# Kernel optimization log

Measured on AMD Instinct MI355X. Metric: run time of the kernel, lower is better.

Reference implementation:

```python
import jax, jax.numpy as jnp
import numpy as np

B, N, M, D = 4096, 39, 32, 32   # batch, fields, embed_dim, product_layer_dim
F = 1_000_000                   # features_dim (sparse vocab)
H = [400, 400, 400]             # hidden layer sizes
BN_EPS = 1e-3                   # keras BatchNormalization default epsilon


def setup_inputs() -> dict:
    key = jax.random.key(0)
    ks = jax.random.split(key, 32)
    inp = {
        "feature_index": jax.random.randint(ks[0], (B, N), 0, F),
        "feature_value": jax.random.normal(ks[1], (B, N), dtype=jnp.float32),
        # keras Embedding default 'uniform' initializer: U(-0.05, 0.05)
        "emb_table": jax.random.uniform(ks[2], (F, M), minval=-0.05, maxval=0.05, dtype=jnp.float32),
        "lin_w": jax.random.normal(ks[3], (D, N, M), dtype=jnp.float32) * 0.05,
        "quad_w": jax.random.normal(ks[4], (D, N), dtype=jnp.float32) * 0.1,
    }
    # MLP: input is concat(l_z, l_p) -> 2*D wide
    dims = [2 * D] + H
    k = 5
    for i in range(len(H)):
        fan_in, fan_out = dims[i], dims[i + 1]
        scale = (2.0 / (fan_in + fan_out)) ** 0.5
        inp[f"W{i}"] = jax.random.normal(ks[k], (fan_in, fan_out), dtype=jnp.float32) * scale; k += 1
        inp[f"b{i}"] = jnp.zeros((fan_out,), jnp.float32)
        inp[f"g{i}"] = jnp.ones((fan_out,), jnp.float32)    # BN gamma
        inp[f"be{i}"] = jnp.zeros((fan_out,), jnp.float32)  # BN beta
        inp[f"rm{i}"] = jnp.zeros((fan_out,), jnp.float32)  # BN moving mean
        inp[f"rv{i}"] = jnp.ones((fan_out,), jnp.float32)   # BN moving var
    inp["Wout"] = jax.random.normal(ks[k], (H[-1], 1), dtype=jnp.float32) * 0.05
    inp["bout"] = jnp.zeros((1,), jnp.float32)
    return inp


def _forward(feature_index, emb_table, lin_w, quad_w, layer_params, Wout, bout):
    e = emb_table[feature_index]                          # (B, N, M) embedding lookup
    l_z = jnp.einsum('bnm,dnm->bd', e, lin_w)             # linear signal
    theta = jnp.einsum('bnm,dn->bdnm', e, quad_w)         # IPNN quadratic signal
    l_p = jnp.einsum('bdnm,bdnm->bd', theta, theta)       # sum of squares over (n, m)
    x = jnp.concatenate([l_z, l_p], axis=1)               # (B, 2D)
    for (W, b, g, be, rm, rv) in layer_params:
        x = x @ W + b
        x = (x - rm) * jax.lax.rsqrt(rv + BN_EPS) * g + be  # BN (inference stats)
        x = jax.nn.relu(x)
    return jax.nn.sigmoid(x @ Wout + bout)                # (B, 1)


def reference(feature_index, feature_value, emb_table, lin_w, quad_w,
              W0, b0, g0, be0, rm0, rv0,
              W1, b1, g1, be1, rm1, rv1,
              W2, b2, g2, be2, rm2, rv2,
              Wout, bout):
    # feature_value is accepted by the original call() but never used; dropout disabled (eval).
    layer_params = [
        (W0, b0, g0, be0, rm0, rv0),
        (W1, b1, g1, be1, rm1, rv1),
        (W2, b2, g2, be2, rm2, rv2),
    ]
    return _forward(feature_index, emb_table, lin_w, quad_w, layer_params, Wout, bout)
```

## Files before the change

### kernel.cpp

```cpp
#include <hip/hip_runtime.h>
#include <hip/hip_bf16.h>
#include <math.h>

#define TB 4096
#define TN 39
#define TM 32
#define TD 32
#define TH 400
#define BN_EPS 1e-3f

#define KT0 2
#define KTH 13

typedef __attribute__((ext_vector_type(8))) short bf16x8;
typedef __attribute__((ext_vector_type(4))) float f32x4;

__device__ __forceinline__ ushort bf16_rn(float x) {
    __hip_bfloat16 h = __float2bfloat16(x);
    union { __hip_bfloat16 b; ushort u; } c; c.b = h; return c.u;
}
__device__ __forceinline__ void split2(float x, ushort& hi, ushort& lo) {
    unsigned xb = __float_as_uint(x);
    unsigned hb = xb & 0xFFFF0000u;
    hi = (ushort)(hb >> 16);
    lo = bf16_rn(x - __uint_as_float(hb));
}

__device__ __forceinline__ void gload_lds16(const ushort* g, ushort* l) {
    __builtin_amdgcn_global_load_lds(
        (const __attribute__((address_space(1))) void*)g,
        (__attribute__((address_space(3))) void*)l,
        16, 0, 0);
}

__device__ __forceinline__ size_t panel_idx(int p, int k, int KT) {
    int lane_ = (p & 15) + 16 * ((k >> 2) & 3);
    int j_    = (k & 3) + 4 * ((k >> 4) & 1);
    return (((size_t)((p >> 4) * KT + (k >> 5)) * 64) + lane_) * 8 + j_;
}

__global__ __launch_bounds__(256) void fused_front_kernel(
    const int*   __restrict__ fidx,
    const float* __restrict__ emb,
    const float* __restrict__ lin_w,
    const float* __restrict__ quad_w,
    const float* __restrict__ W0, const float* __restrict__ W1, const float* __restrict__ W2,
    const float* __restrict__ b0_, const float* __restrict__ g0_, const float* __restrict__ be0_,
    const float* __restrict__ rm0_, const float* __restrict__ rv0_,
    const float* __restrict__ b1_, const float* __restrict__ g1_, const float* __restrict__ be1_,
    const float* __restrict__ rm1_, const float* __restrict__ rv1_,
    const float* __restrict__ b2_, const float* __restrict__ g2_, const float* __restrict__ be2_,
    const float* __restrict__ rm2_, const float* __restrict__ rv2_,
    ushort* __restrict__ A0h, ushort* __restrict__ A0l,
    ushort* __restrict__ B0h, ushort* __restrict__ B0l,
    ushort* __restrict__ B1h, ushort* __restrict__ B1l,
    ushort* __restrict__ B2h, ushort* __restrict__ B2l,
    float* __restrict__ AC)
{
    if (blockIdx.x >= TB / 4) {
        int tid = (blockIdx.x - TB / 4) * 256 + threadIdx.x;
        const int NW0 = 64 * 112, NW = 416 * 112;
        if (tid < NW0 + 2 * NW) {
            const float* W; ushort *Ph, *Pl; int k, n4, K, KT;
            if (tid < NW0) {
                W = W0; Ph = B0h; Pl = B0l; k = tid / 112; n4 = tid % 112; K = 64; KT = KT0;
            } else if (tid < NW0 + NW) {
                int u = tid - NW0;
                W = W1; Ph = B1h; Pl = B1l; k = u / 112; n4 = u % 112; K = TH; KT = KTH;
            } else {
                int u = tid - NW0 - NW;
                W = W2; Ph = B2h; Pl = B2l; k = u / 112; n4 = u % 112; K = TH; KT = KTH;
            }
            int n0 = n4 * 4;
            float4 w = make_float4(0.f, 0.f, 0.f, 0.f);
            if (k < K && n0 < TH)
                w = *(const float4*)&W[(size_t)k * TH + n0];
            float vals[4] = {w.x, w.y, w.z, w.w};
            #pragma unroll
            for (int i = 0; i < 4; ++i) {
                ushort hi, lo; split2(vals[i], hi, lo);
                size_t idx = panel_idx(n0 + i, k, KT);
                Ph[idx] = hi; Pl[idx] = lo;
            }
        } else if (tid < NW0 + 2 * NW + 3 * 448) {
            int u = tid - NW0 - 2 * NW;
            int layer = u / 448, h = u % 448;
            const float *gp, *bep, *rmp, *rvp, *bp;
            if (layer == 0)      { gp = g0_; bep = be0_; rmp = rm0_; rvp = rv0_; bp = b0_; }
            else if (layer == 1) { gp = g1_; bep = be1_; rmp = rm1_; rvp = rv1_; bp = b1_; }
            else                 { gp = g2_; bep = be2_; rmp = rm2_; rvp = rv2_; bp = b2_; }
            float aj = 0.f, cj = 0.f;
            if (h < TH) {
                aj = gp[h] * rsqrtf(rvp[h] + BN_EPS);
                cj = (bp[h] - rmp[h]) * aj + bep[h];
            }
            AC[layer * 896 + h] = aj;
            AC[layer * 896 + 448 + h] = cj;
        }
        return;
    }

    constexpr int R = 4;
    __shared__ float e_s[R][TN * TM];
    __shared__ int   idx_s[R][TN];
    __shared__ float s_s[R][TN];

    const int t  = threadIdx.x;
    const int b0 = blockIdx.x * R;

    if (t < R * TN) {
        int r = t / TN, n = t - r * TN;
        idx_s[r][n] = fidx[(b0 + r) * TN + n];
    }
    __syncthreads();

    for (int r = 0; r < R; ++r) {
        for (int k4 = t; k4 < TN * TM / 4; k4 += 256) {
            int n = k4 >> 3;
            long long base = (long long)idx_s[r][n] * TM + ((k4 & 7) << 2);
            *(float4*)&e_s[r][k4 * 4] = *(const float4*)&emb[base];
        }
    }
    __syncthreads();

    {
        const int d = t >> 3, j = t & 7;
        float acc[R] = {0.f, 0.f, 0.f, 0.f};
        const float* lw_base = lin_w + d * (TN * TM);
        #pragma unroll 4
        for (int i = 0; i < TN; ++i) {
            float4 lw = *(const float4*)&lw_base[i * 32 + j * 4];
            #pragma unroll
            for (int r = 0; r < R; ++r) {
                float4 e4 = *(const float4*)&e_s[r][i * 32 + j * 4];
                acc[r] = fmaf(lw.x, e4.x, acc[r]);
                acc[r] = fmaf(lw.y, e4.y, acc[r]);
                acc[r] = fmaf(lw.z, e4.z, acc[r]);
                acc[r] = fmaf(lw.w, e4.w, acc[r]);
            }
        }
        #pragma unroll
        for (int off = 1; off < 8; off <<= 1)
            #pragma unroll
            for (int r = 0; r < R; ++r)
                acc[r] += __shfl_xor(acc[r], off);
        if (j == 0) {
            #pragma unroll
            for (int r = 0; r < R; ++r) {
                ushort hi, lo; split2(acc[r], hi, lo);
                size_t idx = panel_idx(b0 + r, d, KT0);
                A0h[idx] = hi; A0l[idx] = lo;
            }
        }
    }

    {
        int r = t >> 6, lane = t & 63;
        if (lane < TN) {
            float s = 0.f;
            #pragma unroll
            for (int mm = 0; mm < TM; ++mm) {
                float v = e_s[r][lane * TM + ((lane + mm) & 31)];
                s = fmaf(v, v, s);
            }
            s_s[r][lane] = s;
        }
    }
    __syncthreads();

    if (t < R * TD) {
        int r = t >> 5, d = t & 31;
        float accv = 0.f;
        for (int n = 0; n < TN; ++n) {
            float q = quad_w[d * TN + n];
            accv = fmaf(s_s[r][n], q * q, accv);
        }
        ushort hi, lo; split2(accv, hi, lo);
        size_t idx = panel_idx(b0 + r, TD + d, KT0);
        A0h[idx] = hi; A0l[idx] = lo;
    }
}

template <int KT, int OUTMODE>
__global__ __launch_bounds__(256) void gemm_layer_v7(
    const ushort* __restrict__ Ah, const ushort* __restrict__ Al,
    const ushort* __restrict__ Bh, const ushort* __restrict__ Bl,
    const float* __restrict__ ACl,
    ushort* __restrict__ Nh, ushort* __restrict__ Nl,
    const float* __restrict__ Wout,
    float* __restrict__ P)
{
    __shared__ ushort stage[2][16 * 512];

    const int lane = threadIdx.x & 63;
    const int wv   = threadIdx.x >> 6;
    const int msel = wv >> 1;
    const int nsel = wv & 1;

    const int orig = blockIdx.x;
    const int xcd  = orig & 7;
    const int slot = orig >> 3;
    const int bm   = (slot & 7) * 8 + xcd;
    const int bn   = slot >> 3;

    const ushort* csrc[4];
    int coff[4];
    #pragma unroll
    for (int i = 0; i < 4; ++i) {
        int c = wv * 4 + i;
        bool isA = c < 8;
        int tl  = isA ? (c >> 1) : ((c - 8) >> 1);
        bool lo = c & 1;
        const ushort* base = isA ? (lo ? Al : Ah) : (lo ? Bl : Bh);
        int tileIdx = isA ? (bm * 4 + tl) : (bn * 4 + tl);
        csrc[i] = base + (size_t)tileIdx * KT * 512 + (size_t)lane * 8;
        coff[i] = c * 512;
    }

    f32x4 acc[2][2];
    #pragma unroll
    for (int m = 0; m < 2; ++m)
        #pragma unroll
        for (int n = 0; n < 2; ++n)
            acc[m][n] = (f32x4){0.f, 0.f, 0.f, 0.f};

    #pragma unroll
    for (int i = 0; i < 4; ++i)
        gload_lds16(csrc[i], &stage[0][coff[i]]);
    __syncthreads();

    for (int kt = 0; kt < KT; ++kt) {
        const int cur = kt & 1;
        if (kt + 1 < KT) {
            #pragma unroll
            for (int i = 0; i < 4; ++i)
                gload_lds16(csrc[i] + (size_t)(kt + 1) * 512,
                            &stage[cur ^ 1][coff[i]]);
        }
        const ushort* L = &stage[cur][0];
        bf16x8 ah[2], al[2], bh[2], bl[2];
        #pragma unroll
        for (int m = 0; m < 2; ++m) {
            int mt = msel * 2 + m;
            ah[m] = *(const bf16x8*)&L[(mt * 2 + 0) * 512 + lane * 8];
            al[m] = *(const bf16x8*)&L[(mt * 2 + 1) * 512 + lane * 8];
        }
        #pragma unroll
        for (int n = 0; n < 2; ++n) {
            int nt = nsel * 2 + n;
            bh[n] = *(const bf16x8*)&L[(8 + nt * 2 + 0) * 512 + lane * 8];
            bl[n] = *(const bf16x8*)&L[(8 + nt * 2 + 1) * 512 + lane * 8];
        }
        #pragma unroll
        for (int m = 0; m < 2; ++m)
            #pragma unroll
            for (int n = 0; n < 2; ++n) {
                acc[m][n] = __builtin_amdgcn_mfma_f32_16x16x32_bf16(ah[m], bh[n], acc[m][n], 0, 0, 0);
                acc[m][n] = __builtin_amdgcn_mfma_f32_16x16x32_bf16(ah[m], bl[n], acc[m][n], 0, 0, 0);
                acc[m][n] = __builtin_amdgcn_mfma_f32_16x16x32_bf16(al[m], bh[n], acc[m][n], 0, 0, 0);
            }
        __syncthreads();
    }

    const int col = lane & 15, rq = (lane >> 4) << 2;

    if constexpr (OUTMODE == 0) {
        float (*ysm)[68] = (float (*)[68])(void*)&stage[0][0];
        #pragma unroll
        for (int m = 0; m < 2; ++m)
            #pragma unroll
            for (int n = 0; n < 2; ++n) {
                int h = bn * 64 + (nsel * 2 + n) * 16 + col;
                float aj = ACl[h], cj = ACl[448 + h];
                #pragma unroll
                for (int r = 0; r < 4; ++r)
                    ysm[msel * 32 + m * 16 + rq + r][(nsel * 2 + n) * 16 + col] =
                        fmaxf(fmaf(acc[m][n][r], aj, cj), 0.f);
            }
        __syncthreads();

        const int ck = wv & 1;
        const int kt32 = bn * 2 + ck;
        if (kt32 < KTH) {
            #pragma unroll
            for (int mi = 0; mi < 2; ++mi) {
                int mtl = (wv >> 1) * 2 + mi;
                int row_l = mtl * 16 + (lane & 15);
                int kb = ck * 32 + rq;
                float4 v0 = *(const float4*)&ysm[row_l][kb];
                float4 v1 = *(const float4*)&ysm[row_l][kb + 16];
                ushort h_[8], l_[8];
                split2(v0.x, h_[0], l_[0]); split2(v0.y, h_[1], l_[1]);
                split2(v0.z, h_[2], l_[2]); split2(v0.w, h_[3], l_[3]);
                split2(v1.x, h_[4], l_[4]); split2(v1.y, h_[5], l_[5]);
                split2(v1.z, h_[6], l_[6]); split2(v1.w, h_[7], l_[7]);
                uint4 H, L2;
                H.x = (uint)h_[0] | ((uint)h_[1] << 16);
                H.y = (uint)h_[2] | ((uint)h_[3] << 16);
                H.z = (uint)h_[4] | ((uint)h_[5] << 16);
                H.w = (uint)h_[6] | ((uint)h_[7] << 16);
                L2.x = (uint)l_[0] | ((uint)l_[1] << 16);
                L2.y = (uint)l_[2] | ((uint)l_[3] << 16);
                L2.z = (uint)l_[4] | ((uint)l_[5] << 16);
                L2.w = (uint)l_[6] | ((uint)l_[7] << 16);
                size_t base = (((size_t)(bm * 4 + mtl) * KTH + kt32) * 64 + lane) * 8;
                *(uint4*)(Nh + base) = H;
                *(uint4*)(Nl + base) = L2;
            }
        }
    } else {
        float partial[2][4] = {{0.f,0.f,0.f,0.f},{0.f,0.f,0.f,0.f}};
        #pragma unroll
        for (int m = 0; m < 2; ++m)
            #pragma unroll
            for (int n = 0; n < 2; ++n) {
                int h = bn * 64 + (nsel * 2 + n) * 16 + col;
                float aj = ACl[h], cj = ACl[448 + h];
                float wv_ = (h < TH) ? Wout[h] : 0.f;
                #pragma unroll
                for (int r = 0; r < 4; ++r) {
                    float y = fmaxf(fmaf(acc[m][n][r], aj, cj), 0.f);
                    partial[m][r] = fmaf(y, wv_, partial[m][r]);
                }
            }
        #pragma unroll
        for (int off = 1; off < 16; off <<= 1)
            #pragma unroll
            for (int m = 0; m < 2; ++m)
                #pragma unroll
                for (int r = 0; r < 4; ++r)
                    partial[m][r] += __shfl_xor(partial[m][r], off);
        if (col == 0) {
            #pragma unroll
            for (int m = 0; m < 2; ++m)
                #pragma unroll
                for (int r = 0; r < 4; ++r)
                    P[(size_t)(bm * 64 + msel * 32 + m * 16 + rq + r) * 16
                      + bn * 2 + nsel] = partial[m][r];
        }
    }
}

__global__ __launch_bounds__(256) void fin_kernel(
    const float* __restrict__ P, const float* __restrict__ bout,
    float* __restrict__ out)
{
    int row = blockIdx.x * 256 + threadIdx.x;
    const float4* p = (const float4*)(P + (size_t)row * 16);
    float4 p0 = p[0], p1 = p[1], p2 = p[2], p3 = p[3];
    float s = bout[0]
            + p0.x + p0.y + p0.z + p0.w
            + p1.x + p1.y + p1.z + p1.w
            + p2.x + p2.y + p2.z + p2.w
            + p3.x + p3.y;
    out[row] = 1.f / (1.f + expf(-s));
}

extern "C" void kernel_launch(void* const* d_in, const int* in_sizes, int n_in,
                              void* d_out, int out_size, void* d_ws, size_t ws_size,
                              hipStream_t stream) {
    const int*   fidx   = (const int*)  d_in[0];
    const float* emb    = (const float*)d_in[2];
    const float* lin_w  = (const float*)d_in[3];
    const float* quad_w = (const float*)d_in[4];

    const float* W0  = (const float*)d_in[5];
    const float* b0  = (const float*)d_in[6];
    const float* g0  = (const float*)d_in[7];
    const float* be0 = (const float*)d_in[8];
    const float* rm0 = (const float*)d_in[9];
    const float* rv0 = (const float*)d_in[10];

    const float* W1  = (const float*)d_in[11];
    const float* b1  = (const float*)d_in[12];
    const float* g1  = (const float*)d_in[13];
    const float* be1 = (const float*)d_in[14];
    const float* rm1 = (const float*)d_in[15];
    const float* rv1 = (const float*)d_in[16];

    const float* W2  = (const float*)d_in[17];
    const float* b2  = (const float*)d_in[18];
    const float* g2  = (const float*)d_in[19];
    const float* be2 = (const float*)d_in[20];
    const float* rm2 = (const float*)d_in[21];
    const float* rv2 = (const float*)d_in[22];

    const float* Wout = (const float*)d_in[23];
    const float* bout = (const float*)d_in[24];

    const size_t SZ_A0 = (size_t)256 * KT0 * 512;
    const size_t SZ_A  = (size_t)256 * KTH * 512;
    const size_t SZ_B0 = (size_t)28  * KT0 * 512;
    const size_t SZ_B  = (size_t)28  * KTH * 512;

    ushort* p = (ushort*)d_ws;
    ushort *A0h = p; p += SZ_A0; ushort *A0l = p; p += SZ_A0;
    ushort *A1h = p; p += SZ_A;  ushort *A1l = p; p += SZ_A;
    ushort *A2h = p; p += SZ_A;  ushort *A2l = p; p += SZ_A;
    ushort *B0h = p; p += SZ_B0; ushort *B0l = p; p += SZ_B0;
    ushort *B1h = p; p += SZ_B;  ushort *B1l = p; p += SZ_B;
    ushort *B2h = p; p += SZ_B;  ushort *B2l = p; p += SZ_B;
    float*  AC  = (float*)p;
    float*  Pst = AC + 3 * 896;

    fused_front_kernel<<<TB / 4 + 398, 256, 0, stream>>>(
        fidx, emb, lin_w, quad_w, W0, W1, W2,
        b0, g0, be0, rm0, rv0,
        b1, g1, be1, rm1, rv1,
        b2, g2, be2, rm2, rv2,
        A0h, A0l, B0h, B0l, B1h, B1l, B2h, B2l, AC);

    gemm_layer_v7<KT0, 0><<<448, 256, 0, stream>>>(
        A0h, A0l, B0h, B0l, AC + 0, A1h, A1l, nullptr, nullptr);
    gemm_layer_v7<KTH, 0><<<448, 256, 0, stream>>>(
        A1h, A1l, B1h, B1l, AC + 896, A2h, A2l, nullptr, nullptr);
    gemm_layer_v7<KTH, 1><<<448, 256, 0, stream>>>(
        A2h, A2l, B2h, B2l, AC + 1792, nullptr, nullptr, Wout, Pst);

    fin_kernel<<<TB / 256, 256, 0, stream>>>(Pst, bout, (float*)d_out);
}
```

Before: 47.27 us.

## Fuse three GEMM layers and final sigmoid into one kernel with row-group barriers

Replaces the three per-layer GEMM launches and the finishing kernel with one persistent kernel. Blocks sharing a row tile (7 column blocks) synchronise through atomic counters between layers, and the last block of each row group computes the sigmoid output. Counters are zeroed in the front kernel. This removes launch gaps and the extra final kernel, but relies on all 448 blocks being co-resident (launch bounds 256,2) and adds spin-wait barrier cost.

```diff
diff --git a/kernel.cpp b/kernel.cpp
--- a/kernel.cpp
+++ b/kernel.cpp
@@ -11,6 +11,9 @@
 
 #define KT0 2
 #define KTH 13
+
+#define CNT_STRIDE 32
+#define CNT_TOTAL  (192 * CNT_STRIDE)
 
 typedef __attribute__((ext_vector_type(8))) short bf16x8;
 typedef __attribute__((ext_vector_type(4))) float f32x4;
@@ -55,7 +58,7 @@
     ushort* __restrict__ B0h, ushort* __restrict__ B0l,
     ushort* __restrict__ B1h, ushort* __restrict__ B1l,
     ushort* __restrict__ B2h, ushort* __restrict__ B2l,
-    float* __restrict__ AC)
+    float* __restrict__ AC, int* __restrict__ cnt)
 {
     if (blockIdx.x >= TB / 4) {
         int tid = (blockIdx.x - TB / 4) * 256 + threadIdx.x;
@@ -96,6 +99,8 @@
             }
             AC[layer * 896 + h] = aj;
             AC[layer * 896 + 448 + h] = cj;
+        } else if (tid < NW0 + 2 * NW + 3 * 448 + CNT_TOTAL) {
+            cnt[tid - (NW0 + 2 * NW + 3 * 448)] = 0;
         }
         return;
     }
@@ -182,26 +187,17 @@
 }
 
 template <int KT, int OUTMODE>
-__global__ __launch_bounds__(256) void gemm_layer_v7(
+__device__ __forceinline__ void gemm_body(
     const ushort* __restrict__ Ah, const ushort* __restrict__ Al,
     const ushort* __restrict__ Bh, const ushort* __restrict__ Bl,
     const float* __restrict__ ACl,
     ushort* __restrict__ Nh, ushort* __restrict__ Nl,
-    const float* __restrict__ Wout,
-    float* __restrict__ P)
+    const float* __restrict__ Wout, float* __restrict__ P,
+    ushort (*stage)[16 * 512],
+    int lane, int wv, int bm, int bn)
 {
-    __shared__ ushort stage[2][16 * 512];
-
-    const int lane = threadIdx.x & 63;
-    const int wv   = threadIdx.x >> 6;
     const int msel = wv >> 1;
     const int nsel = wv & 1;
-
-    const int orig = blockIdx.x;
-    const int xcd  = orig & 7;
-    const int slot = orig >> 3;
-    const int bm   = (slot & 7) * 8 + xcd;
-    const int bn   = slot >> 3;
 
     const ushort* csrc[4];
     int coff[4];
@@ -308,6 +304,7 @@
                 *(uint4*)(Nl + base) = L2;
             }
         }
+        __syncthreads();
     } else {
         float partial[2][4] = {{0.f,0.f,0.f,0.f},{0.f,0.f,0.f,0.f}};
         #pragma unroll
@@ -341,19 +338,70 @@
     }
 }
 
-__global__ __launch_bounds__(256) void fin_kernel(
-    const float* __restrict__ P, const float* __restrict__ bout,
-    float* __restrict__ out)
+__device__ __forceinline__ void layer_barrier(int* c) {
+    __syncthreads();
+    if (threadIdx.x == 0) {
+        __threadfence();
+        atomicAdd(c, 1);
+        while (atomicAdd(c, 0) < 7)
+            __builtin_amdgcn_s_sleep(4);
+        __threadfence();
+    }
+    __syncthreads();
+}
+
+__global__ __launch_bounds__(256, 2) void mega_mlp_kernel(
+    const ushort* __restrict__ A0h, const ushort* __restrict__ A0l,
+    ushort* __restrict__ A1h, ushort* __restrict__ A1l,
+    ushort* __restrict__ A2h, ushort* __restrict__ A2l,
+    const ushort* __restrict__ B0h, const ushort* __restrict__ B0l,
+    const ushort* __restrict__ B1h, const ushort* __restrict__ B1l,
+    const ushort* __restrict__ B2h, const ushort* __restrict__ B2l,
+    const float* __restrict__ AC, const float* __restrict__ Wout,
+    const float* __restrict__ bout,
+    float* __restrict__ P, int* __restrict__ cnt, float* __restrict__ out)
 {
-    int row = blockIdx.x * 256 + threadIdx.x;
-    const float4* p = (const float4*)(P + (size_t)row * 16);
-    float4 p0 = p[0], p1 = p[1], p2 = p[2], p3 = p[3];
-    float s = bout[0]
-            + p0.x + p0.y + p0.z + p0.w
-            + p1.x + p1.y + p1.z + p1.w
-            + p2.x + p2.y + p2.z + p2.w
-            + p3.x + p3.y;
-    out[row] = 1.f / (1.f + expf(-s));
+    __shared__ ushort stage[2][16 * 512];
+    __shared__ int sh_last;
+
+    const int lane = threadIdx.x & 63;
+    const int wv   = threadIdx.x >> 6;
+
+    const int orig = blockIdx.x;
+    const int xcd  = orig & 7;
+    const int slot = orig >> 3;
+    const int bm   = (slot & 7) * 8 + xcd;
+    const int bn   = slot >> 3;
+
+    gemm_body<KT0, 0>(A0h, A0l, B0h, B0l, AC + 0, A1h, A1l,
+                      nullptr, nullptr, stage, lane, wv, bm, bn);
+    layer_barrier(&cnt[(0 * 64 + bm) * CNT_STRIDE]);
+
+    gemm_body<KTH, 0>(A1h, A1l, B1h, B1l, AC + 896, A2h, A2l,
+                      nullptr, nullptr, stage, lane, wv, bm, bn);
+    layer_barrier(&cnt[(1 * 64 + bm) * CNT_STRIDE]);
+
+    gemm_body<KTH, 1>(A2h, A2l, B2h, B2l, AC + 1792, nullptr, nullptr,
+                      Wout, P, stage, lane, wv, bm, bn);
+
+    __syncthreads();
+    if (threadIdx.x == 0) {
+        __threadfence();
+        int old = atomicAdd(&cnt[(2 * 64 + bm) * CNT_STRIDE], 1);
+        sh_last = (old == 6);
+    }
+    __syncthreads();
+    if (sh_last) {
+        __threadfence();
+        int t = threadIdx.x;
+        if (t < 64) {
+            const float* pr = P + (size_t)(bm * 64 + t) * 16;
+            float s = bout[0];
+            #pragma unroll
+            for (int i = 0; i < 14; ++i) s += pr[i];
+            out[bm * 64 + t] = 1.f / (1.f + expf(-s));
+        }
+    }
 }
 
 extern "C" void kernel_launch(void* const* d_in, const int* in_sizes, int n_in,
@@ -402,20 +450,17 @@
     ushort *B2h = p; p += SZ_B;  ushort *B2l = p; p += SZ_B;
     float*  AC  = (float*)p;
     float*  Pst = AC + 3 * 896;
-
-    fused_front_kernel<<<TB / 4 + 398, 256, 0, stream>>>(
+    int*    cnt = (int*)(Pst + (size_t)TB * 16);
+
+    fused_front_kernel<<<TB / 4 + 422, 256, 0, stream>>>(
         fidx, emb, lin_w, quad_w, W0, W1, W2,
         b0, g0, be0, rm0, rv0,
         b1, g1, be1, rm1, rv1,
         b2, g2, be2, rm2, rv2,
-        A0h, A0l, B0h, B0l, B1h, B1l, B2h, B2l, AC);
-
-    gemm_layer_v7<KT0, 0><<<448, 256, 0, stream>>>(
-        A0h, A0l, B0h, B0l, AC + 0, A1h, A1l, nullptr, nullptr);
-    gemm_layer_v7<KTH, 0><<<448, 256, 0, stream>>>(
-        A1h, A1l, B1h, B1l, AC + 896, A2h, A2l, nullptr, nullptr);
-    gemm_layer_v7<KTH, 1><<<448, 256, 0, stream>>>(
-        A2h, A2l, B2h, B2l, AC + 1792, nullptr, nullptr, Wout, Pst);
-
-    fin_kernel<<<TB / 256, 256, 0, stream>>>(Pst, bout, (float*)d_out);
-}
+        A0h, A0l, B0h, B0l, B1h, B1l, B2h, B2l, AC, cnt);
+
+    mega_mlp_kernel<<<448, 256, 0, stream>>>(
+        A0h, A0l, A1h, A1l, A2h, A2l,
+        B0h, B0l, B1h, B1l, B2h, B2l,
+        AC, Wout, bout, Pst, cnt, (float*)d_out);
+}
```

Result: slower. 108.2 us (+129.0%).
